# Kernel optimization log

Measured on AMD Instinct MI355X. Metric: run time of the kernel, lower is better.

Reference implementation:

```python
import jax, jax.numpy as jnp
import numpy as np

T = 5          # Newton iterations (init kwarg T)
EPS = 1e-05    # covariance regularizer (init kwarg eps)


def setup_inputs() -> dict:
    key = jax.random.key(0)
    k1, k2 = jax.random.split(key)
    B, C, H, W = 64, 128, 56, 56
    x = jax.random.normal(k1, (B, C, H, W), dtype=jnp.float32)
    running_rot = jax.random.normal(k2, (C, C), dtype=jnp.float32)
    return {"x": x, "running_rot": running_rot}


def reference(x, running_rot):
    # Concept Whitening forward (training-mode batch statistics), channels_first.
    # 1) IterNorm ZCA whitening via T Newton iterations on the CxC covariance.
    # 2) Rotation by the (non-trainable) running rotation matrix.
    B, C, H, W = x.shape
    m = B * H * W
    # (C, m): channels as rows, all samples/locations as columns
    xt = x.transpose(1, 0, 2, 3).reshape(C, m)
    mean = jnp.mean(xt, axis=1, keepdims=True)
    xc = xt - mean
    I = jnp.eye(C, dtype=x.dtype)
    Sigma = EPS * I + (xc @ xc.T) / m            # (C, C)
    rTr = 1.0 / jnp.trace(Sigma)                 # trace normalization
    SigmaN = Sigma * rTr
    P = I
    for _ in range(T):                           # Newton iteration for Sigma^{-1/2}
        P = 0.5 * (3.0 * P - P @ P @ P @ SigmaN)
    wm = P * jnp.sqrt(rTr)                       # whitening matrix Sigma^{-1/2}
    xn = wm @ xc                                 # whitened activations (C, m)
    x_hat = xn.reshape(C, B, H, W).transpose(1, 0, 2, 3)  # (B, C, H, W)
    # rotate into concept-aligned basis: out[b,d,h,w] = sum_c rot[d,c] * x_hat[b,c,h,w]
    out = jnp.einsum('bchw,dc->bdhw', x_hat, running_rot)
    return out
```

## Files before the change

### kernel.cpp

```cpp
#include <hip/hip_runtime.h>
#include <math.h>

#define HW 3136
#define NCHUNK 3136
#define M_TOT 200704.0f
#define EPSV 1e-5f

typedef __attribute__((ext_vector_type(8))) short bf16x8;
typedef __attribute__((ext_vector_type(4))) short short4v;
typedef __attribute__((ext_vector_type(4))) float f32x4;

__device__ inline unsigned short f2bf(float f) {
  unsigned u = __float_as_uint(f);
  u += 0x7FFFu + ((u >> 16) & 1u);
  return (unsigned short)(u >> 16);
}

__global__ __launch_bounds__(512, 4) void gram_k(const float* __restrict__ x,
                                                 float* __restrict__ partG,
                                                 float* __restrict__ partS,
                                                 int slots) {
  __shared__ unsigned short xs[2][128 * 72];
  const int t = threadIdx.x;
  const int lm = t & 15, quad = (t >> 4) & 3, w = t >> 6;
  const int row0 = w * 16;
  const int qofs = (t & 15) * 4;
  const int chi = t >> 4;

  f32x4 acc[8];
  f32x4 sacc;
  const f32x4 z = {0.f, 0.f, 0.f, 0.f};
  sacc = z;
#pragma unroll
  for (int j = 0; j < 8; ++j) acc[j] = z;
  bf16x8 ones;
#pragma unroll
  for (int j = 0; j < 8; ++j) ones[j] = (short)0x3F80;

  int chunk = blockIdx.x;
  float4 pre[4];
  {
    const int b = chunk / 49;
    const int s0 = (chunk % 49) * 64;
    const float* base = x + (size_t)(b * 128) * HW + s0;
#pragma unroll
    for (int i = 0; i < 4; ++i)
      pre[i] = *(const float4*)(base + (size_t)(i * 32 + chi) * HW + qofs);
  }

  int buf = 0;
  while (chunk < NCHUNK) {
#pragma unroll
    for (int i = 0; i < 4; ++i) {
      const int c = i * 32 + chi;
      uint2 dw;
      dw.x = (unsigned)f2bf(pre[i].x) | ((unsigned)f2bf(pre[i].y) << 16);
      dw.y = (unsigned)f2bf(pre[i].z) | ((unsigned)f2bf(pre[i].w) << 16);
      *(uint2*)&xs[buf][c * 72 + qofs] = dw;
    }
    __syncthreads();
    const int nxt = chunk + slots;
    if (nxt < NCHUNK) {
      const int b = nxt / 49;
      const int s0 = (nxt % 49) * 64;
      const float* base = x + (size_t)(b * 128) * HW + s0;
#pragma unroll
      for (int i = 0; i < 4; ++i)
        pre[i] = *(const float4*)(base + (size_t)(i * 32 + chi) * HW + qofs);
    }
#pragma unroll
    for (int ks = 0; ks < 2; ++ks) {
      const int ko = ks * 32 + quad * 8;
      const bf16x8 a0 = *(const bf16x8*)&xs[buf][(row0 + lm) * 72 + ko];
      sacc = __builtin_amdgcn_mfma_f32_16x16x32_bf16(a0, ones, sacc, 0, 0, 0);
#pragma unroll
      for (int tj = 0; tj < 8; ++tj) {
        const bf16x8 bf = *(const bf16x8*)&xs[buf][(tj * 16 + lm) * 72 + ko];
        acc[tj] = __builtin_amdgcn_mfma_f32_16x16x32_bf16(a0, bf, acc[tj], 0, 0, 0);
      }
    }
    buf ^= 1;
    chunk = nxt;
  }

  float* pg = partG + (size_t)blockIdx.x * 16384;
#pragma unroll
  for (int tj = 0; tj < 8; ++tj)
#pragma unroll
    for (int r = 0; r < 4; ++r)
      pg[(row0 + quad * 4 + r) * 128 + tj * 16 + lm] = acc[tj][r];
  if (lm == 0) {
#pragma unroll
    for (int r = 0; r < 4; ++r)
      partS[blockIdx.x * 128 + row0 + quad * 4 + r] = sacc[r];
  }
}

__global__ __launch_bounds__(256) void reduce1_k(const float* __restrict__ partG,
                                                 const float* __restrict__ partS,
                                                 float* __restrict__ part2,
                                                 float* __restrict__ part2S,
                                                 int slots) {
  const int t = threadIdx.x;
  const int sg = blockIdx.x & 31;
  const int eg = blockIdx.x >> 5;
  const int e4 = eg * 1024 + t * 4;
  float ax = 0.f, ay = 0.f, az = 0.f, aw = 0.f;
#pragma unroll 4
  for (int s = sg; s < slots; s += 32) {
    const float4 v = *(const float4*)(partG + (size_t)s * 16384 + e4);
    ax += v.x; ay += v.y; az += v.z; aw += v.w;
  }
  *(float4*)(part2 + (size_t)sg * 16384 + e4) = make_float4(ax, ay, az, aw);
  if (eg == 0 && t < 128) {
    float sa = 0.f;
    for (int s = sg; s < slots; s += 32) sa += partS[s * 128 + t];
    part2S[sg * 128 + t] = sa;
  }
}

__global__ __launch_bounds__(256) void sigred_k(const float* __restrict__ part2,
                                                const float* __restrict__ part2S,
                                                float* __restrict__ Sigma,
                                                float* __restrict__ traceP,
                                                float* __restrict__ meanOut) {
  __shared__ float SbL[128];
  __shared__ float red[256];
  const int t = threadIdx.x;
  if (t < 128) {
    float sa = 0.f;
#pragma unroll
    for (int sg = 0; sg < 32; ++sg) sa += part2S[sg * 128 + t];
    SbL[t] = sa;
    if (blockIdx.x == 0) meanOut[t] = sa * (1.0f / M_TOT);
  }
  __syncthreads();
  const int e4 = blockIdx.x * 1024 + t * 4;
  float ax = 0.f, ay = 0.f, az = 0.f, aw = 0.f;
#pragma unroll
  for (int sg = 0; sg < 32; ++sg) {
    const float4 v = *(const float4*)(part2 + (size_t)sg * 16384 + e4);
    ax += v.x; ay += v.y; az += v.z; aw += v.w;
  }
  const int r = e4 >> 7, c0 = e4 & 127;
  const float rm = 1.0f / M_TOT;
  const float sr = SbL[r] * rm;
  float s4[4];
  s4[0] = (ax - sr * SbL[c0 + 0]) * rm;
  s4[1] = (ay - sr * SbL[c0 + 1]) * rm;
  s4[2] = (az - sr * SbL[c0 + 2]) * rm;
  s4[3] = (aw - sr * SbL[c0 + 3]) * rm;
  float trl = 0.f;
#pragma unroll
  for (int j = 0; j < 4; ++j) {
    if (c0 + j == r) { s4[j] += EPSV; trl = s4[j]; }
  }
  *(float4*)(Sigma + e4) = make_float4(s4[0], s4[1], s4[2], s4[3]);
  red[t] = trl;
  __syncthreads();
  for (int off = 128; off > 0; off >>= 1) {
    if (t < off) red[t] += red[t + off];
    __syncthreads();
  }
  if (t == 0) traceP[blockIdx.x] = red[0];
}

__global__ __launch_bounds__(256) void newton1_k(const float* __restrict__ Sig,
                                                 const float* __restrict__ traceP,
                                                 float* __restrict__ Pout) {
  __shared__ float s1[8 * 132];
  __shared__ float s2[8 * 132];
  __shared__ float red[256 * 17];
  const int t = threadIdx.x;
  const int ct = t & 31;
  const int rt = (t >> 5) & 1;
  const int kt = t >> 6;
  const int rg0 = blockIdx.x * 8;
  const int ra = rg0 + 4 * rt;
  float tr = 0.f;
#pragma unroll
  for (int i = 0; i < 16; ++i) tr += traceP[i];
  const float rTr = 1.0f / tr;
  const float nh = -0.5f * rTr;
  float a[4][4];

#pragma unroll
  for (int i = 0; i < 4; ++i)
#pragma unroll
    for (int j = 0; j < 4; ++j) a[i][j] = 0.f;
#pragma unroll 4
  for (int k = kt * 32; k < kt * 32 + 32; ++k) {
    const float4 sa4 = *(const float4*)(Sig + k * 128 + ra);
    const float4 sb4 = *(const float4*)(Sig + k * 128 + 4 * ct);
    float aA[4] = {nh * sa4.x, nh * sa4.y, nh * sa4.z, nh * sa4.w};
    float bA[4] = {nh * sb4.x, nh * sb4.y, nh * sb4.z, nh * sb4.w};
#pragma unroll
    for (int i = 0; i < 4; ++i) if (ra + i == k) aA[i] += 1.5f;
#pragma unroll
    for (int j = 0; j < 4; ++j) if (4 * ct + j == k) bA[j] += 1.5f;
#pragma unroll
    for (int i = 0; i < 4; ++i)
#pragma unroll
      for (int j = 0; j < 4; ++j) a[i][j] += aA[i] * bA[j];
  }
#pragma unroll
  for (int i = 0; i < 4; ++i)
#pragma unroll
    for (int j = 0; j < 4; ++j) red[t * 17 + i * 4 + j] = a[i][j];
  __syncthreads();
  if (t < 64) {
#pragma unroll
    for (int u = 1; u < 4; ++u)
#pragma unroll
      for (int i = 0; i < 4; ++i)
#pragma unroll
        for (int j = 0; j < 4; ++j)
          a[i][j] += red[(t + 64 * u) * 17 + i * 4 + j];
#pragma unroll
    for (int i = 0; i < 4; ++i)
#pragma unroll
      for (int j = 0; j < 4; ++j)
        s1[(4 * rt + i) * 132 + 4 * ct + j] = a[i][j];
  }
  __syncthreads();

#pragma unroll
  for (int i = 0; i < 4; ++i)
#pragma unroll
    for (int j = 0; j < 4; ++j) a[i][j] = 0.f;
#pragma unroll 4
  for (int k = kt * 32; k < kt * 32 + 32; ++k) {
    float aA[4];
#pragma unroll
    for (int i = 0; i < 4; ++i) aA[i] = s1[(4 * rt + i) * 132 + k];
    const float4 sb4 = *(const float4*)(Sig + k * 128 + 4 * ct);
    float bA[4] = {nh * sb4.x, nh * sb4.y, nh * sb4.z, nh * sb4.w};
#pragma unroll
    for (int j = 0; j < 4; ++j) if (4 * ct + j == k) bA[j] += 1.5f;
#pragma unroll
    for (int i = 0; i < 4; ++i)
#pragma unroll
      for (int j = 0; j < 4; ++j) a[i][j] += aA[i] * bA[j];
  }
  __syncthreads();
#pragma unroll
  for (int i = 0; i < 4; ++i)
#pragma unroll
    for (int j = 0; j < 4; ++j) red[t * 17 + i * 4 + j] = a[i][j];
  __syncthreads();
  if (t < 64) {
#pragma unroll
    for (int u = 1; u < 4; ++u)
#pragma unroll
      for (int i = 0; i < 4; ++i)
#pragma unroll
        for (int j = 0; j < 4; ++j)
          a[i][j] += red[(t + 64 * u) * 17 + i * 4 + j];
#pragma unroll
    for (int i = 0; i < 4; ++i)
#pragma unroll
      for (int j = 0; j < 4; ++j)
        s2[(4 * rt + i) * 132 + 4 * ct + j] = a[i][j];
  }
  __syncthreads();

#pragma unroll
  for (int i = 0; i < 4; ++i)
#pragma unroll
    for (int j = 0; j < 4; ++j) a[i][j] = 0.f;
#pragma unroll 4
  for (int k = kt * 32; k < kt * 32 + 32; ++k) {
    float aA[4];
#pragma unroll
    for (int i = 0; i < 4; ++i) aA[i] = s2[(4 * rt + i) * 132 + k];
    const float4 bv = *(const float4*)(Sig + k * 128 + 4 * ct);
    const float bA[4] = {bv.x, bv.y, bv.z, bv.w};
#pragma unroll
    for (int i = 0; i < 4; ++i)
#pragma unroll
      for (int j = 0; j < 4; ++j) a[i][j] += aA[i] * bA[j];
  }
  __syncthreads();
#pragma unroll
  for (int i = 0; i < 4; ++i)
#pragma unroll
    for (int j = 0; j < 4; ++j) red[t * 17 + i * 4 + j] = a[i][j];
  __syncthreads();
  if (t < 64) {
#pragma unroll
    for (int u = 1; u < 4; ++u)
#pragma unroll
      for (int i = 0; i < 4; ++i)
#pragma unroll
        for (int j = 0; j < 4; ++j)
          a[i][j] += red[(t + 64 * u) * 17 + i * 4 + j];
#pragma unroll
    for (int i = 0; i < 4; ++i) {
      const int rg = rg0 + 4 * rt + i;
      const float4 sv = *(const float4*)(Sig + rg * 128 + 4 * ct);
      float p1v[4] = {nh * sv.x, nh * sv.y, nh * sv.z, nh * sv.w};
#pragma unroll
      for (int j = 0; j < 4; ++j) if (4 * ct + j == rg) p1v[j] += 1.5f;
      *(float4*)(Pout + rg * 128 + 4 * ct) =
          make_float4(0.5f * (3.f * p1v[0] - rTr * a[i][0]),
                      0.5f * (3.f * p1v[1] - rTr * a[i][1]),
                      0.5f * (3.f * p1v[2] - rTr * a[i][2]),
                      0.5f * (3.f * p1v[3] - rTr * a[i][3]));
    }
  }
}

__global__ __launch_bounds__(256) void newton_k(const float* __restrict__ P,
                                                const float* __restrict__ Sig,
                                                const float* __restrict__ traceP,
                                                float* __restrict__ Pout) {
  __shared__ float s1[8 * 132];
  __shared__ float s2[8 * 132];
  __shared__ float red[256 * 17];
  const int t = threadIdx.x;
  const int ct = t & 31;
  const int rt = (t >> 5) & 1;
  const int kt = t >> 6;
  const int rg0 = blockIdx.x * 8;
  float tr = 0.f;
#pragma unroll
  for (int i = 0; i < 16; ++i) tr += traceP[i];
  const float rTr = 1.0f / tr;
  float a[4][4];

#pragma unroll
  for (int i = 0; i < 4; ++i)
#pragma unroll
    for (int j = 0; j < 4; ++j) a[i][j] = 0.f;
#pragma unroll 4
  for (int k = kt * 32; k < kt * 32 + 32; ++k) {
    const float4 av = *(const float4*)(P + k * 128 + rg0 + 4 * rt);
    const float4 bv = *(const float4*)(P + k * 128 + 4 * ct);
    const float aA[4] = {av.x, av.y, av.z, av.w};
    const float bA[4] = {bv.x, bv.y, bv.z, bv.w};
#pragma unroll
    for (int i = 0; i < 4; ++i)
#pragma unroll
      for (int j = 0; j < 4; ++j) a[i][j] += aA[i] * bA[j];
  }
#pragma unroll
  for (int i = 0; i < 4; ++i)
#pragma unroll
    for (int j = 0; j < 4; ++j) red[t * 17 + i * 4 + j] = a[i][j];
  __syncthreads();
  if (t < 64) {
#pragma unroll
    for (int u = 1; u < 4; ++u)
#pragma unroll
      for (int i = 0; i < 4; ++i)
#pragma unroll
        for (int j = 0; j < 4; ++j)
          a[i][j] += red[(t + 64 * u) * 17 + i * 4 + j];
#pragma unroll
    for (int i = 0; i < 4; ++i)
#pragma unroll
      for (int j = 0; j < 4; ++j)
        s1[(4 * rt + i) * 132 + 4 * ct + j] = a[i][j];
  }
  __syncthreads();

#pragma unroll
  for (int i = 0; i < 4; ++i)
#pragma unroll
    for (int j = 0; j < 4; ++j) a[i][j] = 0.f;
#pragma unroll 4
  for (int k = kt * 32; k < kt * 32 + 32; ++k) {
    float aA[4];
#pragma unroll
    for (int i = 0; i < 4; ++i) aA[i] = s1[(4 * rt + i) * 132 + k];
    const float4 bv = *(const float4*)(P + k * 128 + 4 * ct);
    const float bA[4] = {bv.x, bv.y, bv.z, bv.w};
#pragma unroll
    for (int i = 0; i < 4; ++i)
#pragma unroll
      for (int j = 0; j < 4; ++j) a[i][j] += aA[i] * bA[j];
  }
  __syncthreads();
#pragma unroll
  for (int i = 0; i < 4; ++i)
#pragma unroll
    for (int j = 0; j < 4; ++j) red[t * 17 + i * 4 + j] = a[i][j];
  __syncthreads();
  if (t < 64) {
#pragma unroll
    for (int u = 1; u < 4; ++u)
#pragma unroll
      for (int i = 0; i < 4; ++i)
#pragma unroll
        for (int j = 0; j < 4; ++j)
          a[i][j] += red[(t + 64 * u) * 17 + i * 4 + j];
#pragma unroll
    for (int i = 0; i < 4; ++i)
#pragma unroll
      for (int j = 0; j < 4; ++j)
        s2[(4 * rt + i) * 132 + 4 * ct + j] = a[i][j];
  }
  __syncthreads();

#pragma unroll
  for (int i = 0; i < 4; ++i)
#pragma unroll
    for (int j = 0; j < 4; ++j) a[i][j] = 0.f;
#pragma unroll 4
  for (int k = kt * 32; k < kt * 32 + 32; ++k) {
    float aA[4];
#pragma unroll
    for (int i = 0; i < 4; ++i) aA[i] = s2[(4 * rt + i) * 132 + k];
    const float4 bv = *(const float4*)(Sig + k * 128 + 4 * ct);
    const float bA[4] = {bv.x, bv.y, bv.z, bv.w};
#pragma unroll
    for (int i = 0; i < 4; ++i)
#pragma unroll
      for (int j = 0; j < 4; ++j) a[i][j] += aA[i] * bA[j];
  }
  __syncthreads();
#pragma unroll
  for (int i = 0; i < 4; ++i)
#pragma unroll
    for (int j = 0; j < 4; ++j) red[t * 17 + i * 4 + j] = a[i][j];
  __syncthreads();
  if (t < 64) {
#pragma unroll
    for (int u = 1; u < 4; ++u)
#pragma unroll
      for (int i = 0; i < 4; ++i)
#pragma unroll
        for (int j = 0; j < 4; ++j)
          a[i][j] += red[(t + 64 * u) * 17 + i * 4 + j];
#pragma unroll
    for (int i = 0; i < 4; ++i) {
      const int rg = rg0 + 4 * rt + i;
      const float4 pv = *(const float4*)(P + rg * 128 + 4 * ct);
      *(float4*)(Pout + rg * 128 + 4 * ct) =
          make_float4(0.5f * (3.f * pv.x - rTr * a[i][0]),
                      0.5f * (3.f * pv.y - rTr * a[i][1]),
                      0.5f * (3.f * pv.z - rTr * a[i][2]),
                      0.5f * (3.f * pv.w - rTr * a[i][3]));
    }
  }
}

__global__ __launch_bounds__(256) void rotmt_k(const float* __restrict__ rot,
                                               const float* __restrict__ P,
                                               const float* __restrict__ mean,
                                               const float* __restrict__ traceP,
                                               unsigned short* __restrict__ Mbf,
                                               float* __restrict__ bias) {
  const int t = threadIdx.x;
  const int r = t >> 5;
  const int dg = blockIdx.x * 8 + r;
  const int c0 = (t & 31) * 4;
  const float* rrow = rot + dg * 128;
  float tr = 0.f;
#pragma unroll
  for (int i = 0; i < 16; ++i) tr += traceP[i];
  const float sc = sqrtf(1.0f / tr);

  float ax = 0, ay = 0, az = 0, aw = 0;
#pragma unroll 4
  for (int k = 0; k < 128; ++k) {
    const float a = rrow[k];
    const float4 bv = *(const float4*)(P + k * 128 + c0);
    ax += a * bv.x; ay += a * bv.y; az += a * bv.z; aw += a * bv.w;
  }
  ax *= sc; ay *= sc; az *= sc; aw *= sc;
  uint2 dw;
  dw.x = (unsigned)f2bf(ax) | ((unsigned)f2bf(ay) << 16);
  dw.y = (unsigned)f2bf(az) | ((unsigned)f2bf(aw) << 16);
  *(uint2*)&Mbf[dg * 128 + c0] = dw;
  const float4 mv = *(const float4*)(mean + c0);
  float p = ax * mv.x + ay * mv.y + az * mv.z + aw * mv.w;
  for (int off = 16; off > 0; off >>= 1) p += __shfl_down(p, off, 32);
  if ((t & 31) == 0) bias[dg] = p;
}

#define MSTR 136
#define XSTR 132
__global__ __launch_bounds__(256, 2) void apply_k(const float* __restrict__ x,
                                                  const unsigned short* __restrict__ Mbf,
                                                  const float* __restrict__ bias,
                                                  float* __restrict__ out) {
  __shared__ unsigned short Ms[128 * MSTR];
  __shared__ unsigned short xsB[64 * XSTR];
  const int t = threadIdx.x;
  const int lm = t & 15, quad = (t >> 4) & 3, w = t >> 6;
  const int b = blockIdx.x / 49;
  const int s0 = (blockIdx.x % 49) * 64;

#pragma unroll
  for (int i = 0; i < 8; ++i) {
    const int e = i * 256 + t;
    const int row = e >> 4, oct = e & 15;
    *(uint4*)&Ms[row * MSTR + oct * 8] =
        *(const uint4*)(Mbf + row * 128 + oct * 8);
  }
#pragma unroll
  for (int i = 0; i < 4; ++i) {
    const int p = 16 * i + (t >> 4);
    const int q = t & 15;
    const float* px = x + (size_t)(b * 128 + 2 * p) * HW + s0 + 4 * q;
    const float4 fa = *(const float4*)px;
    const float4 fb = *(const float4*)(px + HW);
    const float faA[4] = {fa.x, fa.y, fa.z, fa.w};
    const float fbA[4] = {fb.x, fb.y, fb.z, fb.w};
#pragma unroll
    for (int r = 0; r < 4; ++r) {
      const unsigned dw =
          (unsigned)f2bf(faA[r]) | ((unsigned)f2bf(fbA[r]) << 16);
      *(unsigned*)&xsB[(4 * q + r) * XSTR + 2 * p] = dw;
    }
  }
  float biasr[2][4];
#pragma unroll
  for (int i = 0; i < 2; ++i)
#pragma unroll
    for (int r = 0; r < 4; ++r)
      biasr[i][r] = bias[(2 * w + i) * 16 + quad * 4 + r];
  __syncthreads();

  const f32x4 z = {0.f, 0.f, 0.f, 0.f};
  f32x4 acc[2][4];
#pragma unroll
  for (int i = 0; i < 2; ++i)
#pragma unroll
    for (int sj = 0; sj < 4; ++sj) acc[i][sj] = z;

#pragma unroll
  for (int ks = 0; ks < 4; ++ks) {
    const int ko = ks * 32 + quad * 8;
    const bf16x8 a0 = *(const bf16x8*)&Ms[((2 * w + 0) * 16 + lm) * MSTR + ko];
    const bf16x8 a1 = *(const bf16x8*)&Ms[((2 * w + 1) * 16 + lm) * MSTR + ko];
#pragma unroll
    for (int sj = 0; sj < 4; ++sj) {
      const short4v blo = *(const short4v*)&xsB[(sj * 16 + lm) * XSTR + ko];
      const short4v bhi = *(const short4v*)&xsB[(sj * 16 + lm) * XSTR + ko + 4];
      const bf16x8 bf = __builtin_shufflevector(blo, bhi, 0, 1, 2, 3, 4, 5, 6, 7);
      acc[0][sj] = __builtin_amdgcn_mfma_f32_16x16x32_bf16(a0, bf, acc[0][sj], 0, 0, 0);
      acc[1][sj] = __builtin_amdgcn_mfma_f32_16x16x32_bf16(a1, bf, acc[1][sj], 0, 0, 0);
    }
  }
#pragma unroll
  for (int i = 0; i < 2; ++i)
#pragma unroll
    for (int r = 0; r < 4; ++r) {
      const int d = (2 * w + i) * 16 + quad * 4 + r;
      float* orow = out + (size_t)(b * 128 + d) * HW + s0 + lm;
#pragma unroll
      for (int sj = 0; sj < 4; ++sj)
        orow[sj * 16] = acc[i][sj][r] - biasr[i][r];
    }
}

extern "C" void kernel_launch(void* const* d_in, const int* in_sizes, int n_in,
                              void* d_out, int out_size, void* d_ws,
                              size_t ws_size, hipStream_t stream) {
  const float* x = (const float*)d_in[0];
  const float* rot = (const float*)d_in[1];
  float* out = (float*)d_out;
  float* ws = (float*)d_ws;

  float* Sigma  = ws;
  float* Pa     = ws + 16384;
  float* Pb     = ws + 32768;
  unsigned short* Mbf = (unsigned short*)(ws + 49152);
  float* Sb     = ws + 57344;
  float* bias   = ws + 57472;
  float* traceP = ws + 57600;
  float* part2  = ws + 57616;
  float* part2S = ws + 57616 + 524288;
  float* partG  = ws + 57616 + 524288 + 4096;

  const size_t wsf = ws_size / 4;
  long avail = (long)wsf - (57616 + 524288 + 4096);
  int slots = (int)(avail / (16384 + 128));
  if (slots > 512) slots = 512;
  if (slots < 1) slots = 1;
  float* partS = partG + (size_t)slots * 16384;

  gram_k<<<slots, 512, 0, stream>>>(x, partG, partS, slots);
  reduce1_k<<<512, 256, 0, stream>>>(partG, partS, part2, part2S, slots);
  sigred_k<<<16, 256, 0, stream>>>(part2, part2S, Sigma, traceP, Sb);
  newton1_k<<<16, 256, 0, stream>>>(Sigma, traceP, Pb);
  newton_k<<<16, 256, 0, stream>>>(Pb, Sigma, traceP, Pa);
  newton_k<<<16, 256, 0, stream>>>(Pa, Sigma, traceP, Pb);
  newton_k<<<16, 256, 0, stream>>>(Pb, Sigma, traceP, Pa);
  rotmt_k<<<16, 256, 0, stream>>>(rot, Pa, Sb, traceP, Mbf, bias);
  apply_k<<<3136, 256, 0, stream>>>(x, Mbf, bias, out);
}
```

Baseline: 264.4 us.

## Fuse two-stage Gram reduction into one kernel, atomics for sums and trace

The two-level reduction of per-block partial Gram matrices (reduce1_k plus sigred_k) is replaced by a single gsig_k kernel with one block per Sigma row, removing a kernel launch and an intermediate buffer round trip. Channel sums and the trace are now accumulated with atomicAdd into a memset-cleared buffer. The Newton kernels double their thread count so each thread covers half the k-range, apply_k's occupancy hint rises from 2 to 3 blocks per CU, and the mean is folded into rotmt_k. The atomics make float summation order nondeterministic, and gsig_k reads 512 slot strides per row, which may give less coalesced access.

Result: slower. 299.6 us (+13.3%).

```diff
diff --git a/kernel.cpp b/kernel.cpp
--- a/kernel.cpp
+++ b/kernel.cpp
@@ -18,7 +18,7 @@
 
 __global__ __launch_bounds__(512, 4) void gram_k(const float* __restrict__ x,
                                                  float* __restrict__ partG,
-                                                 float* __restrict__ partS,
+                                                 float* __restrict__ S,
                                                  int slots) {
   __shared__ unsigned short xs[2][128 * 72];
   const int t = threadIdx.x;
@@ -92,95 +92,72 @@
   if (lm == 0) {
 #pragma unroll
     for (int r = 0; r < 4; ++r)
-      partS[blockIdx.x * 128 + row0 + quad * 4 + r] = sacc[r];
-  }
-}
-
-__global__ __launch_bounds__(256) void reduce1_k(const float* __restrict__ partG,
-                                                 const float* __restrict__ partS,
-                                                 float* __restrict__ part2,
-                                                 float* __restrict__ part2S,
-                                                 int slots) {
+      atomicAdd(&S[row0 + quad * 4 + r], sacc[r]);
+  }
+}
+
+__global__ __launch_bounds__(256) void gsig_k(const float* __restrict__ partG,
+                                              const float* __restrict__ S,
+                                              float* __restrict__ Sigma,
+                                              float* __restrict__ trace,
+                                              int slots) {
+  __shared__ float4 red[256];
   const int t = threadIdx.x;
-  const int sg = blockIdx.x & 31;
-  const int eg = blockIdx.x >> 5;
-  const int e4 = eg * 1024 + t * 4;
+  const int q = t & 31;
+  const int h = t >> 5;
+  const int b = blockIdx.x;
+  const float* base = partG + (size_t)b * 128 + 4 * q;
   float ax = 0.f, ay = 0.f, az = 0.f, aw = 0.f;
-#pragma unroll 4
-  for (int s = sg; s < slots; s += 32) {
-    const float4 v = *(const float4*)(partG + (size_t)s * 16384 + e4);
+#pragma unroll 8
+  for (int s = h; s < slots; s += 8) {
+    const float4 v = *(const float4*)(base + (size_t)s * 16384);
     ax += v.x; ay += v.y; az += v.z; aw += v.w;
   }
-  *(float4*)(part2 + (size_t)sg * 16384 + e4) = make_float4(ax, ay, az, aw);
-  if (eg == 0 && t < 128) {
-    float sa = 0.f;
-    for (int s = sg; s < slots; s += 32) sa += partS[s * 128 + t];
-    part2S[sg * 128 + t] = sa;
-  }
-}
-
-__global__ __launch_bounds__(256) void sigred_k(const float* __restrict__ part2,
-                                                const float* __restrict__ part2S,
-                                                float* __restrict__ Sigma,
-                                                float* __restrict__ traceP,
-                                                float* __restrict__ meanOut) {
-  __shared__ float SbL[128];
-  __shared__ float red[256];
-  const int t = threadIdx.x;
+  red[t] = make_float4(ax, ay, az, aw);
+  __syncthreads();
   if (t < 128) {
-    float sa = 0.f;
-#pragma unroll
-    for (int sg = 0; sg < 32; ++sg) sa += part2S[sg * 128 + t];
-    SbL[t] = sa;
-    if (blockIdx.x == 0) meanOut[t] = sa * (1.0f / M_TOT);
-  }
-  __syncthreads();
-  const int e4 = blockIdx.x * 1024 + t * 4;
-  float ax = 0.f, ay = 0.f, az = 0.f, aw = 0.f;
-#pragma unroll
-  for (int sg = 0; sg < 32; ++sg) {
-    const float4 v = *(const float4*)(part2 + (size_t)sg * 16384 + e4);
-    ax += v.x; ay += v.y; az += v.z; aw += v.w;
-  }
-  const int r = e4 >> 7, c0 = e4 & 127;
-  const float rm = 1.0f / M_TOT;
-  const float sr = SbL[r] * rm;
-  float s4[4];
-  s4[0] = (ax - sr * SbL[c0 + 0]) * rm;
-  s4[1] = (ay - sr * SbL[c0 + 1]) * rm;
-  s4[2] = (az - sr * SbL[c0 + 2]) * rm;
-  s4[3] = (aw - sr * SbL[c0 + 3]) * rm;
-  float trl = 0.f;
-#pragma unroll
-  for (int j = 0; j < 4; ++j) {
-    if (c0 + j == r) { s4[j] += EPSV; trl = s4[j]; }
-  }
-  *(float4*)(Sigma + e4) = make_float4(s4[0], s4[1], s4[2], s4[3]);
-  red[t] = trl;
-  __syncthreads();
-  for (int off = 128; off > 0; off >>= 1) {
-    if (t < off) red[t] += red[t + off];
-    __syncthreads();
-  }
-  if (t == 0) traceP[blockIdx.x] = red[0];
-}
-
-__global__ __launch_bounds__(256) void newton1_k(const float* __restrict__ Sig,
-                                                 const float* __restrict__ traceP,
+    const float4 o = red[t + 128];
+    red[t].x += o.x; red[t].y += o.y; red[t].z += o.z; red[t].w += o.w;
+  }
+  __syncthreads();
+  if (t < 64) {
+    const float4 o = red[t + 64];
+    red[t].x += o.x; red[t].y += o.y; red[t].z += o.z; red[t].w += o.w;
+  }
+  __syncthreads();
+  if (t < 32) {
+    const float4 g0 = red[t];
+    const float4 g1 = red[t + 32];
+    const float rm = 1.0f / M_TOT;
+    const float sb = S[b] * rm;
+    const float4 s4 = *(const float4*)(S + 4 * t);
+    float o[4];
+    o[0] = (g0.x + g1.x - sb * s4.x) * rm;
+    o[1] = (g0.y + g1.y - sb * s4.y) * rm;
+    o[2] = (g0.z + g1.z - sb * s4.z) * rm;
+    o[3] = (g0.w + g1.w - sb * s4.w) * rm;
+    if (t == (b >> 2)) {
+      o[b & 3] += EPSV;
+      atomicAdd(trace, o[b & 3]);
+    }
+    *(float4*)(Sigma + b * 128 + 4 * t) = make_float4(o[0], o[1], o[2], o[3]);
+  }
+}
+
+__global__ __launch_bounds__(512) void newton1_k(const float* __restrict__ Sig,
+                                                 const float* __restrict__ trace,
                                                  float* __restrict__ Pout) {
   __shared__ float s1[8 * 132];
   __shared__ float s2[8 * 132];
-  __shared__ float red[256 * 17];
+  __shared__ float red[512 * 17];
   const int t = threadIdx.x;
   const int ct = t & 31;
   const int rt = (t >> 5) & 1;
   const int kt = t >> 6;
+  const int k0 = kt * 16;
   const int rg0 = blockIdx.x * 8;
   const int ra = rg0 + 4 * rt;
-  float tr = 0.f;
-#pragma unroll
-  for (int i = 0; i < 16; ++i) tr += traceP[i];
-  const float rTr = 1.0f / tr;
+  const float rTr = 1.0f / *trace;
   const float nh = -0.5f * rTr;
   float a[4][4];
 
@@ -189,7 +166,7 @@
 #pragma unroll
     for (int j = 0; j < 4; ++j) a[i][j] = 0.f;
 #pragma unroll 4
-  for (int k = kt * 32; k < kt * 32 + 32; ++k) {
+  for (int k = k0; k < k0 + 16; ++k) {
     const float4 sa4 = *(const float4*)(Sig + k * 128 + ra);
     const float4 sb4 = *(const float4*)(Sig + k * 128 + 4 * ct);
     float aA[4] = {nh * sa4.x, nh * sa4.y, nh * sa4.z, nh * sa4.w};
@@ -210,7 +187,7 @@
   __syncthreads();
   if (t < 64) {
 #pragma unroll
-    for (int u = 1; u < 4; ++u)
+    for (int u = 1; u < 8; ++u)
 #pragma unroll
       for (int i = 0; i < 4; ++i)
 #pragma unroll
@@ -229,7 +206,7 @@
 #pragma unroll
     for (int j = 0; j < 4; ++j) a[i][j] = 0.f;
 #pragma unroll 4
-  for (int k = kt * 32; k < kt * 32 + 32; ++k) {
+  for (int k = k0; k < k0 + 16; ++k) {
     float aA[4];
 #pragma unroll
     for (int i = 0; i < 4; ++i) aA[i] = s1[(4 * rt + i) * 132 + k];
@@ -250,7 +227,7 @@
   __syncthreads();
   if (t < 64) {
 #pragma unroll
-    for (int u = 1; u < 4; ++u)
+    for (int u = 1; u < 8; ++u)
 #pragma unroll
       for (int i = 0; i < 4; ++i)
 #pragma unroll
@@ -269,7 +246,7 @@
 #pragma unroll
     for (int j = 0; j < 4; ++j) a[i][j] = 0.f;
 #pragma unroll 4
-  for (int k = kt * 32; k < kt * 32 + 32; ++k) {
+  for (int k = k0; k < k0 + 16; ++k) {
     float aA[4];
 #pragma unroll
     for (int i = 0; i < 4; ++i) aA[i] = s2[(4 * rt + i) * 132 + k];
@@ -288,7 +265,7 @@
   __syncthreads();
   if (t < 64) {
 #pragma unroll
-    for (int u = 1; u < 4; ++u)
+    for (int u = 1; u < 8; ++u)
 #pragma unroll
       for (int i = 0; i < 4; ++i)
 #pragma unroll
@@ -310,22 +287,20 @@
   }
 }
 
-__global__ __launch_bounds__(256) void newton_k(const float* __restrict__ P,
+__global__ __launch_bounds__(512) void newton_k(const float* __restrict__ P,
                                                 const float* __restrict__ Sig,
-                                                const float* __restrict__ traceP,
+                                                const float* __restrict__ trace,
                                                 float* __restrict__ Pout) {
   __shared__ float s1[8 * 132];
   __shared__ float s2[8 * 132];
-  __shared__ float red[256 * 17];
+  __shared__ float red[512 * 17];
   const int t = threadIdx.x;
   const int ct = t & 31;
   const int rt = (t >> 5) & 1;
   const int kt = t >> 6;
+  const int k0 = kt * 16;
   const int rg0 = blockIdx.x * 8;
-  float tr = 0.f;
-#pragma unroll
-  for (int i = 0; i < 16; ++i) tr += traceP[i];
-  const float rTr = 1.0f / tr;
+  const float rTr = 1.0f / *trace;
   float a[4][4];
 
 #pragma unroll
@@ -333,7 +308,7 @@
 #pragma unroll
     for (int j = 0; j < 4; ++j) a[i][j] = 0.f;
 #pragma unroll 4
-  for (int k = kt * 32; k < kt * 32 + 32; ++k) {
+  for (int k = k0; k < k0 + 16; ++k) {
     const float4 av = *(const float4*)(P + k * 128 + rg0 + 4 * rt);
     const float4 bv = *(const float4*)(P + k * 128 + 4 * ct);
     const float aA[4] = {av.x, av.y, av.z, av.w};
@@ -350,7 +325,7 @@
   __syncthreads();
   if (t < 64) {
 #pragma unroll
-    for (int u = 1; u < 4; ++u)
+    for (int u = 1; u < 8; ++u)
 #pragma unroll
       for (int i = 0; i < 4; ++i)
 #pragma unroll
@@ -369,7 +344,7 @@
 #pragma unroll
     for (int j = 0; j < 4; ++j) a[i][j] = 0.f;
 #pragma unroll 4
-  for (int k = kt * 32; k < kt * 32 + 32; ++k) {
+  for (int k = k0; k < k0 + 16; ++k) {
     float aA[4];
 #pragma unroll
     for (int i = 0; i < 4; ++i) aA[i] = s1[(4 * rt + i) * 132 + k];
@@ -388,7 +363,7 @@
   __syncthreads();
   if (t < 64) {
 #pragma unroll
-    for (int u = 1; u < 4; ++u)
+    for (int u = 1; u < 8; ++u)
 #pragma unroll
       for (int i = 0; i < 4; ++i)
 #pragma unroll
@@ -407,7 +382,7 @@
 #pragma unroll
     for (int j = 0; j < 4; ++j) a[i][j] = 0.f;
 #pragma unroll 4
-  for (int k = kt * 32; k < kt * 32 + 32; ++k) {
+  for (int k = k0; k < k0 + 16; ++k) {
     float aA[4];
 #pragma unroll
     for (int i = 0; i < 4; ++i) aA[i] = s2[(4 * rt + i) * 132 + k];
@@ -426,7 +401,7 @@
   __syncthreads();
   if (t < 64) {
 #pragma unroll
-    for (int u = 1; u < 4; ++u)
+    for (int u = 1; u < 8; ++u)
 #pragma unroll
       for (int i = 0; i < 4; ++i)
 #pragma unroll
@@ -447,8 +422,8 @@
 
 __global__ __launch_bounds__(256) void rotmt_k(const float* __restrict__ rot,
                                                const float* __restrict__ P,
-                                               const float* __restrict__ mean,
-                                               const float* __restrict__ traceP,
+                                               const float* __restrict__ S,
+                                               const float* __restrict__ trace,
                                                unsigned short* __restrict__ Mbf,
                                                float* __restrict__ bias) {
   const int t = threadIdx.x;
@@ -456,10 +431,7 @@
   const int dg = blockIdx.x * 8 + r;
   const int c0 = (t & 31) * 4;
   const float* rrow = rot + dg * 128;
-  float tr = 0.f;
-#pragma unroll
-  for (int i = 0; i < 16; ++i) tr += traceP[i];
-  const float sc = sqrtf(1.0f / tr);
+  const float sc = sqrtf(1.0f / *trace);
 
   float ax = 0, ay = 0, az = 0, aw = 0;
 #pragma unroll 4
@@ -473,15 +445,15 @@
   dw.x = (unsigned)f2bf(ax) | ((unsigned)f2bf(ay) << 16);
   dw.y = (unsigned)f2bf(az) | ((unsigned)f2bf(aw) << 16);
   *(uint2*)&Mbf[dg * 128 + c0] = dw;
-  const float4 mv = *(const float4*)(mean + c0);
-  float p = ax * mv.x + ay * mv.y + az * mv.z + aw * mv.w;
+  const float4 sv = *(const float4*)(S + c0);
+  float p = (ax * sv.x + ay * sv.y + az * sv.z + aw * sv.w) * (1.0f / M_TOT);
   for (int off = 16; off > 0; off >>= 1) p += __shfl_down(p, off, 32);
   if ((t & 31) == 0) bias[dg] = p;
 }
 
 #define MSTR 136
 #define XSTR 132
-__global__ __launch_bounds__(256, 2) void apply_k(const float* __restrict__ x,
+__global__ __launch_bounds__(256, 3) void apply_k(const float* __restrict__ x,
                                                   const unsigned short* __restrict__ Mbf,
                                                   const float* __restrict__ bias,
                                                   float* __restrict__ out) {
@@ -568,27 +540,25 @@
   float* Pa     = ws + 16384;
   float* Pb     = ws + 32768;
   unsigned short* Mbf = (unsigned short*)(ws + 49152);
-  float* Sb     = ws + 57344;
-  float* bias   = ws + 57472;
-  float* traceP = ws + 57600;
-  float* part2  = ws + 57616;
-  float* part2S = ws + 57616 + 524288;
-  float* partG  = ws + 57616 + 524288 + 4096;
+  float* S      = ws + 57344;
+  float* trace  = ws + 57472;
+  float* bias   = ws + 57488;
+  float* partG  = ws + 57616;
 
   const size_t wsf = ws_size / 4;
-  long avail = (long)wsf - (57616 + 524288 + 4096);
-  int slots = (int)(avail / (16384 + 128));
+  long avail = (long)wsf - 57616;
+  int slots = (int)(avail / 16384);
   if (slots > 512) slots = 512;
   if (slots < 1) slots = 1;
-  float* partS = partG + (size_t)slots * 16384;
-
-  gram_k<<<slots, 512, 0, stream>>>(x, partG, partS, slots);
-  reduce1_k<<<512, 256, 0, stream>>>(partG, partS, part2, part2S, slots);
-  sigred_k<<<16, 256, 0, stream>>>(part2, part2S, Sigma, traceP, Sb);
-  newton1_k<<<16, 256, 0, stream>>>(Sigma, traceP, Pb);
-  newton_k<<<16, 256, 0, stream>>>(Pb, Sigma, traceP, Pa);
-  newton_k<<<16, 256, 0, stream>>>(Pa, Sigma, traceP, Pb);
-  newton_k<<<16, 256, 0, stream>>>(Pb, Sigma, traceP, Pa);
-  rotmt_k<<<16, 256, 0, stream>>>(rot, Pa, Sb, traceP, Mbf, bias);
+
+  hipMemsetAsync(S, 0, 129 * 4, stream);
+
+  gram_k<<<slots, 512, 0, stream>>>(x, partG, S, slots);
+  gsig_k<<<128, 256, 0, stream>>>(partG, S, Sigma, trace, slots);
+  newton1_k<<<16, 512, 0, stream>>>(Sigma, trace, Pb);
+  newton_k<<<16, 512, 0, stream>>>(Pb, Sigma, trace, Pa);
+  newton_k<<<16, 512, 0, stream>>>(Pa, Sigma, trace, Pb);
+  newton_k<<<16, 512, 0, stream>>>(Pb, Sigma, trace, Pa);
+  rotmt_k<<<16, 256, 0, stream>>>(rot, Pa, S, trace, Mbf, bias);
   apply_k<<<3136, 256, 0, stream>>>(x, Mbf, bias, out);
 }
```

## Use 224-column chunks in gram kernel and raise apply occupancy hint

Applied to the files above, without the earlier changes.

The gram kernel now loads 224-column chunks (896 chunks total) into a single shared buffer, replacing 64-column double-buffered chunks. Each thread issues 14 float4 loads at once, and the number of blocks is capped at 896 instead of 512. This gives more memory-level parallelism per iteration and fewer loop trips. The cost is dropping the software prefetch overlap, adding an extra barrier per chunk, and using more registers. The apply kernel's launch bounds hint is also raised to 3 blocks per CU.

Measured after the change: 297.3 us. 1.12x slower.

```diff
diff --git a/kernel.cpp b/kernel.cpp
--- a/kernel.cpp
+++ b/kernel.cpp
@@ -2,7 +2,7 @@
 #include <math.h>
 
 #define HW 3136
-#define NCHUNK 3136
+#define NCH224 896
 #define M_TOT 200704.0f
 #define EPSV 1e-5f
 
@@ -20,12 +20,10 @@
                                                  float* __restrict__ partG,
                                                  float* __restrict__ partS,
                                                  int slots) {
-  __shared__ unsigned short xs[2][128 * 72];
+  __shared__ unsigned short xs[128 * 232];
   const int t = threadIdx.x;
   const int lm = t & 15, quad = (t >> 4) & 3, w = t >> 6;
   const int row0 = w * 16;
-  const int qofs = (t & 15) * 4;
-  const int chi = t >> 4;
 
   f32x4 acc[8];
   f32x4 sacc;
@@ -37,50 +35,43 @@
 #pragma unroll
   for (int j = 0; j < 8; ++j) ones[j] = (short)0x3F80;
 
-  int chunk = blockIdx.x;
-  float4 pre[4];
-  {
-    const int b = chunk / 49;
-    const int s0 = (chunk % 49) * 64;
+  for (int chunk = blockIdx.x; chunk < NCH224; chunk += slots) {
+    const int b = chunk / 14;
+    const int s0 = (chunk % 14) * 224;
     const float* base = x + (size_t)(b * 128) * HW + s0;
-#pragma unroll
-    for (int i = 0; i < 4; ++i)
-      pre[i] = *(const float4*)(base + (size_t)(i * 32 + chi) * HW + qofs);
-  }
-
-  int buf = 0;
-  while (chunk < NCHUNK) {
-#pragma unroll
-    for (int i = 0; i < 4; ++i) {
-      const int c = i * 32 + chi;
+
+    float4 buf[14];
+#pragma unroll
+    for (int i = 0; i < 14; ++i) {
+      const int id = t + i * 512;
+      const int c = id / 56;
+      const int qi = id - c * 56;
+      buf[i] = *(const float4*)(base + (size_t)c * HW + 4 * qi);
+    }
+#pragma unroll
+    for (int i = 0; i < 14; ++i) {
+      const int id = t + i * 512;
+      const int c = id / 56;
+      const int qi = id - c * 56;
       uint2 dw;
-      dw.x = (unsigned)f2bf(pre[i].x) | ((unsigned)f2bf(pre[i].y) << 16);
-      dw.y = (unsigned)f2bf(pre[i].z) | ((unsigned)f2bf(pre[i].w) << 16);
-      *(uint2*)&xs[buf][c * 72 + qofs] = dw;
+      dw.x = (unsigned)f2bf(buf[i].x) | ((unsigned)f2bf(buf[i].y) << 16);
+      dw.y = (unsigned)f2bf(buf[i].z) | ((unsigned)f2bf(buf[i].w) << 16);
+      *(uint2*)&xs[c * 232 + 4 * qi] = dw;
     }
     __syncthreads();
-    const int nxt = chunk + slots;
-    if (nxt < NCHUNK) {
-      const int b = nxt / 49;
-      const int s0 = (nxt % 49) * 64;
-      const float* base = x + (size_t)(b * 128) * HW + s0;
-#pragma unroll
-      for (int i = 0; i < 4; ++i)
-        pre[i] = *(const float4*)(base + (size_t)(i * 32 + chi) * HW + qofs);
-    }
-#pragma unroll
-    for (int ks = 0; ks < 2; ++ks) {
+
+#pragma unroll
+    for (int ks = 0; ks < 7; ++ks) {
       const int ko = ks * 32 + quad * 8;
-      const bf16x8 a0 = *(const bf16x8*)&xs[buf][(row0 + lm) * 72 + ko];
+      const bf16x8 a0 = *(const bf16x8*)&xs[(row0 + lm) * 232 + ko];
       sacc = __builtin_amdgcn_mfma_f32_16x16x32_bf16(a0, ones, sacc, 0, 0, 0);
 #pragma unroll
       for (int tj = 0; tj < 8; ++tj) {
-        const bf16x8 bf = *(const bf16x8*)&xs[buf][(tj * 16 + lm) * 72 + ko];
+        const bf16x8 bf = *(const bf16x8*)&xs[(tj * 16 + lm) * 232 + ko];
         acc[tj] = __builtin_amdgcn_mfma_f32_16x16x32_bf16(a0, bf, acc[tj], 0, 0, 0);
       }
     }
-    buf ^= 1;
-    chunk = nxt;
+    __syncthreads();
   }
 
   float* pg = partG + (size_t)blockIdx.x * 16384;
@@ -481,7 +472,7 @@
 
 #define MSTR 136
 #define XSTR 132
-__global__ __launch_bounds__(256, 2) void apply_k(const float* __restrict__ x,
+__global__ __launch_bounds__(256, 3) void apply_k(const float* __restrict__ x,
                                                   const unsigned short* __restrict__ Mbf,
                                                   const float* __restrict__ bias,
                                                   float* __restrict__ out) {
@@ -578,7 +569,7 @@
   const size_t wsf = ws_size / 4;
   long avail = (long)wsf - (57616 + 524288 + 4096);
   int slots = (int)(avail / (16384 + 128));
-  if (slots > 512) slots = 512;
+  if (slots > NCH224) slots = NCH224;
   if (slots < 1) slots = 1;
   float* partS = partG + (size_t)slots * 16384;
 
```
